# Optimization experiments

Measured on AMD Instinct MI355X. Metric: run time of the kernel, lower is better.

The kernel has to match this reference:

```python
import jax, jax.numpy as jnp
import numpy as np

N, C, D, H, E, M = 4, 512, 768, 12, 20, 4   # docs, seq, hidden, heads, entities/doc, max mentions
EMB, BLK, L = 768, 64, 97                    # emb_size, block_size, num_labels
P = E * (E - 1)                              # ordered entity pairs per doc
NEG = -1e30


def _forward(seq, attn, mention_start, hts, Wm1, Wm2, bm, Watt, batt, Wpath, bpath,
             Whead, bhead, Wtail, btail, Wbil, bbil):
    def per_doc(seq_i, att_i, pos0, ht):
        pos = pos0 + 1                                            # BERT cls offset
        e_emb = seq_i[pos]                                        # [E,M,D] mention embeddings
        mean_att = att_i.mean(0)                                  # [C,C] head-mean attention
        e_att = jnp.pad(mean_att[pos], ((0, 0), (0, 0), (0, 1)))  # [E,M,C+1] zero pad col
        glob = jax.nn.logsumexp(e_emb, axis=1)                    # [E,D] entity glob emb
        hidx, tidx = ht[:, 0], ht[:, 1]
        hs = e_emb[hidx]; ts = e_emb[tidx]                        # [P,M,D]
        h_att = e_att[hidx]; t_att = e_att[tidx]                  # [P,M,C+1]
        ph = pos[hidx]; pt = pos[tidx]                            # [P,M]
        idx_t = jnp.broadcast_to(pt[:, None, :], (P, M, M))
        idx_h = jnp.broadcast_to(ph[:, None, :], (P, M, M))
        pair_hatt = jnp.take_along_axis(h_att, idx_t, axis=2).mean(1)  # [P,M]
        pair_tatt = jnp.take_along_axis(t_att, idx_h, axis=2).mean(1)
        pair_hatt = pair_hatt / (pair_hatt.sum(1, keepdims=True) + 1e-5)
        pair_tatt = pair_tatt / (pair_tatt.sum(1, keepdims=True) + 1e-5)
        new_hs = jnp.einsum('pm,pmd->pd', pair_tatt, hs)
        new_ts = jnp.einsum('pm,pmd->pd', pair_hatt, ts)
        nh_att = jnp.einsum('pm,pmc->pc', pair_tatt, h_att)
        nt_att = jnp.einsum('pm,pmc->pc', pair_hatt, t_att)
        pa = nh_att * nt_att
        pa = pa / (pa.sum(1, keepdims=True) + 1e-5)
        rs = pa[:, :C] @ seq_i                                    # [P,D] local context
        # RelEdgeLayer over fully-connected entity graph (eval-mode dropout = identity)
        A = glob @ Wm1; B = glob @ Wm2
        edge = jax.nn.relu(A[:, None, :] + B[None, :, :] + bm)    # [E,E,D] edge features
        # path attention: query = cat(hs,ts), targets = cat(e[h,v],e[v,t],e[t,v],e[v,h])
        q = jnp.concatenate([new_hs, new_ts], -1)                 # [P,2D]
        qW = q @ Watt                                             # [P,4D] bilinear half
        q1, q2, q3, q4 = jnp.split(qW, 4, axis=-1)
        E1 = edge[hidx]                                           # edge[h,v]  [P,E,D]
        E2 = jnp.swapaxes(edge[:, tidx], 0, 1)                    # edge[v,t]
        E3 = edge[tidx]                                           # edge[t,v]
        E4 = jnp.swapaxes(edge[:, hidx], 0, 1)                    # edge[v,h]
        score = (jnp.einsum('pd,pvd->pv', q1, E1) + jnp.einsum('pd,pvd->pv', q2, E2)
                 + jnp.einsum('pd,pvd->pv', q3, E3) + jnp.einsum('pd,pvd->pv', q4, E4) + batt)
        v_ids = jnp.arange(E)
        mask = (v_ids[None, :] == hidx[:, None]) | (v_ids[None, :] == tidx[:, None])
        aw = jax.nn.softmax(jnp.where(mask, NEG, score), axis=-1)  # [P,E]
        path = jnp.concatenate([jnp.einsum('pv,pvd->pd', aw, Ek) for Ek in (E1, E2, E3, E4)], -1)
        return new_hs, new_ts, rs, path

    nh, nt, rs, path = jax.vmap(per_doc)(seq, attn, mention_start, hts)
    nh = nh.reshape(-1, D); nt = nt.reshape(-1, D)
    rs = rs.reshape(-1, D); path = path.reshape(-1, 4 * D)
    path = jax.nn.relu(path @ Wpath + bpath)
    hs = jax.nn.relu(jnp.concatenate([nh, rs, path], -1) @ Whead + bhead)
    ts = jax.nn.relu(jnp.concatenate([nt, rs, path], -1) @ Wtail + btail)
    b1 = hs.reshape(-1, EMB // BLK, BLK)
    b2 = ts.reshape(-1, EMB // BLK, BLK)
    bl = (b1[:, :, :, None] * b2[:, :, None, :]).reshape(-1, EMB * BLK)
    return bl @ Wbil + bbil                                       # [N*P, L] logits


def setup_inputs() -> dict:
    key = jax.random.key(0)
    ks = jax.random.split(key, 16)
    s = 0.02
    pairs = np.array([(i, j) for i in range(E) for j in range(E) if i != j], dtype=np.int32)
    return {
        'sequence_output': jax.random.normal(ks[0], (N, C, D), jnp.float32),
        'attention': jax.random.uniform(ks[1], (N, H, C, C), jnp.float32),
        'mention_start': jax.random.randint(ks[2], (N, E, M), 0, C - 2),
        'hts': jnp.broadcast_to(jnp.asarray(pairs), (N, P, 2)),
        'Wm1': jax.random.normal(ks[3], (D, D)) * s,
        'Wm2': jax.random.normal(ks[4], (D, D)) * s,
        'bm': jnp.zeros((D,), jnp.float32),
        'Watt': jax.random.normal(ks[5], (2 * D, 4 * D)) * s,
        'batt': jnp.zeros((), jnp.float32),
        'Wpath': jax.random.normal(ks[6], (4 * D, D)) * s,
        'bpath': jnp.zeros((D,), jnp.float32),
        'Whead': jax.random.normal(ks[7], (3 * D, EMB)) * s,
        'bhead': jnp.zeros((EMB,), jnp.float32),
        'Wtail': jax.random.normal(ks[8], (3 * D, EMB)) * s,
        'btail': jnp.zeros((EMB,), jnp.float32),
        'Wbil': jax.random.normal(ks[9], (EMB * BLK, L)) * s,
        'bbil': jnp.zeros((L,), jnp.float32),
    }


def reference(sequence_output, attention, mention_start, hts, Wm1, Wm2, bm, Watt, batt,
              Wpath, bpath, Whead, bhead, Wtail, btail, Wbil, bbil):
    return _forward(sequence_output, attention, mention_start, hts, Wm1, Wm2, bm, Watt,
                    batt, Wpath, bpath, Whead, bhead, Wtail, btail, Wbil, bbil)
```

## Files before the change

### kernel.cpp

```cpp
#include <hip/hip_runtime.h>
#include <hip/hip_bf16.h>

#define NDOC 4
#define CL   512
#define DD   768
#define HH   12
#define EE   20
#define MM   4
#define PP   380
#define NPAIR 1520
#define LOUT 97
#define KP   40

typedef unsigned short u16;
typedef short bf16x8 __attribute__((ext_vector_type(8)));
typedef u16   u16x8  __attribute__((ext_vector_type(8)));
typedef u16   u16x4  __attribute__((ext_vector_type(4)));
typedef float f32x4  __attribute__((ext_vector_type(4)));

#define Z8 (u16x8){0,0,0,0,0,0,0,0}

__device__ __forceinline__ u16 f2bf(float x){
    union { float f; unsigned u; } v; v.f = x;
    return (u16)((v.u + 0x7fffu + ((v.u >> 16) & 1u)) >> 16);
}
__device__ __forceinline__ float bf2f(u16 h){
    union { unsigned u; float f; } v; v.u = ((unsigned)h) << 16;
    return v.f;
}
__device__ __forceinline__ void splitf(float x, u16 &h, u16 &l){
    h = f2bf(x);
    l = f2bf(x - bf2f(h));
}
__device__ __forceinline__ void splitf_trunc(float x, u16 &h, u16 &l){
    union { float f; unsigned u; } v; v.f = x;
    h = (u16)(v.u >> 16);
    union { unsigned u; float f; } w; w.u = v.u & 0xffff0000u;
    union { float f; unsigned u; } s; s.f = x - w.f;
    l = (u16)(s.u >> 16);
}

__global__ __launch_bounds__(256) void k_wsplit(const float* __restrict__ W,
                                                u16* __restrict__ WH, u16* __restrict__ WL,
                                                int K, int N, long long srcStride,
                                                long long dstStride)
{
    __shared__ u16 tH[64][66], tL[64][66];
    const float* Wp = W + (size_t)blockIdx.z*srcStride;
    u16* WHp = WH + (size_t)blockIdx.z*dstStride;
    u16* WLp = WL + (size_t)blockIdx.z*dstStride;
    int n0 = blockIdx.x*64, k0 = blockIdx.y*64;
    int t = threadIdx.x;
    int kr = t>>4, c4 = (t&15)*4;
    bool vec4 = ((N & 3) == 0);
    #pragma unroll
    for (int rr=0; rr<4; ++rr) {
        int k = k0 + kr + rr*16;
        float arr[4];
        if (vec4 && n0 + c4 + 3 < N) {
            float4 v = *(const float4*)(Wp + (size_t)k*N + n0 + c4);
            arr[0]=v.x; arr[1]=v.y; arr[2]=v.z; arr[3]=v.w;
        } else {
            #pragma unroll
            for (int i=0;i<4;++i){ int n=n0+c4+i; arr[i] = (n<N)? Wp[(size_t)k*N+n] : 0.f; }
        }
        #pragma unroll
        for (int i=0;i<4;++i){
            u16 hh,ll; splitf(arr[i],hh,ll);
            tH[c4+i][kr+rr*16] = hh;
            tL[c4+i][kr+rr*16] = ll;
        }
    }
    __syncthreads();
    int nr = t>>4, kc = (t&15)*4;
    #pragma unroll
    for (int rr=0; rr<4; ++rr) {
        int nl = nr + rr*16;
        u16x4 vh, vl;
        #pragma unroll
        for (int i=0;i<4;++i){ vh[i]=tH[nl][kc+i]; vl[i]=tL[nl][kc+i]; }
        size_t o = (size_t)(n0+nl)*K + k0 + kc;
        *(u16x4*)(WHp + o) = vh;
        *(u16x4*)(WLp + o) = vl;
    }
}

__global__ __launch_bounds__(256) void k_prep(const float* __restrict__ att,
                                              const float* __restrict__ seq,
                                              const int* __restrict__ ms,
                                              float* __restrict__ eatt,
                                              float* __restrict__ glob)
{
    int b = blockIdx.x;
    if (b < NDOC*EE*MM) {
        int row = b;
        int i = row / (EE*MM);
        int pos = ms[row] + 1;
        const float* base = att + ((size_t)i*HH)*CL*CL + (size_t)pos*CL;
        for (int c = threadIdx.x; c < CL; c += 256) {
            float s = 0.f;
            #pragma unroll
            for (int h = 0; h < HH; ++h) s += base[(size_t)h*CL*CL + c];
            eatt[(size_t)row*CL + c] = s * (1.0f/HH);
        }
    } else {
        int ie = b - NDOC*EE*MM;
        int i = ie / EE;
        const int* mp = ms + ie*MM;
        const float* sb = seq + (size_t)i*CL*DD;
        const float* r0 = sb + (size_t)(mp[0]+1)*DD;
        const float* r1 = sb + (size_t)(mp[1]+1)*DD;
        const float* r2 = sb + (size_t)(mp[2]+1)*DD;
        const float* r3 = sb + (size_t)(mp[3]+1)*DD;
        for (int d = threadIdx.x; d < DD; d += 256) {
            float a=r0[d], bb=r1[d], c=r2[d], e=r3[d];
            float mx = fmaxf(fmaxf(a,bb), fmaxf(c,e));
            float s = expf(a-mx)+expf(bb-mx)+expf(c-mx)+expf(e-mx);
            glob[(size_t)ie*DD + d] = mx + logf(s);
        }
    }
}

__global__ __launch_bounds__(256) void k_pairvec(const float* __restrict__ seq,
                                                 const float* __restrict__ eatt,
                                                 const int* __restrict__ ms,
                                                 const int* __restrict__ hts,
                                                 u16* __restrict__ nhH, u16* __restrict__ nhL,
                                                 u16* __restrict__ ntH, u16* __restrict__ ntL,
                                                 u16* __restrict__ paH, u16* __restrict__ paL)
{
    int g = blockIdx.x;
    int i = g / PP;
    int h = hts[2*g], t = hts[2*g+1];
    const float* eh = eatt + (size_t)(i*EE+h)*MM*CL;
    const float* et = eatt + (size_t)(i*EE+t)*MM*CL;
    int ph[MM], pt[MM];
    #pragma unroll
    for (int m=0;m<MM;++m){ ph[m]=ms[(i*EE+h)*MM+m]+1; pt[m]=ms[(i*EE+t)*MM+m]+1; }
    float pH[MM], pT[MM]; float sh=0.f, st=0.f;
    #pragma unroll
    for (int m2=0; m2<MM; ++m2) {
        float s = 0.f, s2 = 0.f;
        #pragma unroll
        for (int m=0;m<MM;++m) { s += eh[m*CL + pt[m2]]; s2 += et[m*CL + ph[m2]]; }
        pH[m2] = s*0.25f;  sh += pH[m2];
        pT[m2] = s2*0.25f; st += pT[m2];
    }
    float rh = 1.f/(sh+1e-5f), rt = 1.f/(st+1e-5f);
    #pragma unroll
    for (int m=0;m<MM;++m){ pH[m]*=rh; pT[m]*=rt; }

    const float* sb = seq + (size_t)i*CL*DD;
    for (int d = threadIdx.x; d < DD; d += 256) {
        float nh = pT[0]*sb[(size_t)ph[0]*DD+d] + pT[1]*sb[(size_t)ph[1]*DD+d]
                 + pT[2]*sb[(size_t)ph[2]*DD+d] + pT[3]*sb[(size_t)ph[3]*DD+d];
        float nt = pH[0]*sb[(size_t)pt[0]*DD+d] + pH[1]*sb[(size_t)pt[1]*DD+d]
                 + pH[2]*sb[(size_t)pt[2]*DD+d] + pH[3]*sb[(size_t)pt[3]*DD+d];
        u16 hh,ll;
        splitf(nh,hh,ll);
        nhH[(size_t)g*DD + d]=hh; nhL[(size_t)g*DD + d]=ll;
        splitf(nt,hh,ll);
        ntH[(size_t)g*DD + d]=hh; ntL[(size_t)g*DD + d]=ll;
    }
    float vv[2]; float lsum = 0.f;
    #pragma unroll
    for (int it=0; it<2; ++it) {
        int c = threadIdx.x + it*256;
        float na = pT[0]*eh[c] + pT[1]*eh[CL+c] + pT[2]*eh[2*CL+c] + pT[3]*eh[3*CL+c];
        float nb = pH[0]*et[c] + pH[1]*et[CL+c] + pH[2]*et[2*CL+c] + pH[3]*et[3*CL+c];
        vv[it] = na*nb; lsum += vv[it];
    }
    float tot = lsum;
    #pragma unroll
    for (int o=32;o;o>>=1) tot += __shfl_xor(tot, o);
    __shared__ float wsum[4];
    if ((threadIdx.x & 63)==0) wsum[threadIdx.x>>6] = tot;
    __syncthreads();
    float inv = 1.f/(wsum[0]+wsum[1]+wsum[2]+wsum[3] + 1e-5f);
    #pragma unroll
    for (int it=0; it<2; ++it){
        int c = threadIdx.x + it*256;
        u16 hh,ll; splitf(vv[it]*inv,hh,ll);
        paH[(size_t)g*CL + c]=hh; paL[(size_t)g*CL + c]=ll;
    }
}

__global__ __launch_bounds__(256) void k_edge(const float* __restrict__ Ab,
                                              const float* __restrict__ Bb,
                                              const float* __restrict__ bm,
                                              float* __restrict__ edge)
{
    int iht = blockIdx.x;
    int i = iht/(EE*EE); int rem = iht%(EE*EE); int h = rem/EE; int tt = rem%EE;
    const float* a = Ab + (size_t)(i*EE+h)*DD;
    const float* b = Bb + (size_t)(i*EE+tt)*DD;
    float* e = edge + (size_t)iht*DD;
    for (int d=threadIdx.x; d<DD; d+=256)
        e[d] = fmaxf(a[d]+b[d]+bm[d], 0.f);
}

__global__ __launch_bounds__(256) void k_scorepath(const float* __restrict__ qW,
                                                   const float* __restrict__ edge,
                                                   const int* __restrict__ hts,
                                                   const float* __restrict__ battp,
                                                   u16* __restrict__ pathcH,
                                                   u16* __restrict__ pathcL)
{
    int g = blockIdx.x;
    int i = g / PP;
    int h = hts[2*g], t = hts[2*g+1];
    __shared__ float qs[4*DD];
    __shared__ float sc[EE];
    __shared__ float aw[EE];
    for (int d4 = threadIdx.x; d4 < DD; d4 += 256)
        *(float4*)&qs[d4*4] = *(const float4*)(qW + (size_t)g*3072 + d4*4);
    __syncthreads();
    const float* eb = edge + (size_t)i*EE*EE*DD;
    int lane = threadIdx.x & 63, wid = threadIdx.x >> 6;
    for (int v = wid; v < EE; v += 4) {
        const float* e1 = eb + (size_t)(h*EE+v)*DD;
        const float* e2 = eb + (size_t)(v*EE+t)*DD;
        const float* e3 = eb + (size_t)(t*EE+v)*DD;
        const float* e4 = eb + (size_t)(v*EE+h)*DD;
        float s = 0.f;
        for (int d = lane; d < DD; d += 64)
            s += qs[d]*e1[d] + qs[DD+d]*e2[d] + qs[2*DD+d]*e3[d] + qs[3*DD+d]*e4[d];
        #pragma unroll
        for (int o=32;o;o>>=1) s += __shfl_xor(s, o);
        if (lane==0) sc[v] = s + battp[0];
    }
    __syncthreads();
    if (threadIdx.x == 0) {
        float mx = -3.0e38f;
        for (int v=0;v<EE;++v){ float x = (v==h||v==t)? -1e30f : sc[v]; sc[v]=x; mx = fmaxf(mx,x); }
        float su=0.f;
        for (int v=0;v<EE;++v){ float e = expf(sc[v]-mx); aw[v]=e; su+=e; }
        float inv = 1.f/su;
        for (int v=0;v<EE;++v) aw[v]*=inv;
    }
    __syncthreads();
    for (int idx = threadIdx.x; idx < 4*DD; idx += 256) {
        int k = idx / DD, d = idx % DD;
        const float* e;
        int stride;
        if (k==0)      { e = eb + (size_t)h*EE*DD + d; stride = DD; }
        else if (k==1) { e = eb + (size_t)t*DD + d;     stride = EE*DD; }
        else if (k==2) { e = eb + (size_t)t*EE*DD + d;  stride = DD; }
        else           { e = eb + (size_t)h*DD + d;     stride = EE*DD; }
        float s = 0.f;
        #pragma unroll
        for (int v=0; v<EE; ++v) s += aw[v]*e[(size_t)v*stride];
        u16 hh,ll; splitf(s,hh,ll);
        pathcH[(size_t)g*3072 + idx] = hh;
        pathcL[(size_t)g*3072 + idx] = ll;
    }
}

__global__ __launch_bounds__(256) void gemm_f32s(const float* __restrict__ A, int lda, long long sA,
                                                 const float* __restrict__ B, int ldb,
                                                 float* __restrict__ C, int ldc, long long sC,
                                                 int M, int N, int K)
{
    int bz = blockIdx.z;
    A += (size_t)bz*sA;  C += (size_t)bz*sC;
    __shared__ float As[16][68];
    __shared__ float Bs[16][68];
    int m0 = blockIdx.y*64, n0 = blockIdx.x*64;
    int t = threadIdx.x;
    int tx = t & 15, ty = t >> 4;
    int am = t >> 2, ac = (t & 3) * 4;
    int bk = t >> 4, bn = (t & 15) * 4;
    float acc[4][4] = {};
    for (int k0 = 0; k0 < K; k0 += 16) {
        float4 av = make_float4(0,0,0,0);
        int gm = m0 + am;
        if (gm < M) av = *reinterpret_cast<const float4*>(A + (size_t)gm*lda + k0 + ac);
        As[ac+0][am]=av.x; As[ac+1][am]=av.y; As[ac+2][am]=av.z; As[ac+3][am]=av.w;
        float4 bv = *reinterpret_cast<const float4*>(B + (size_t)(k0+bk)*ldb + n0 + bn);
        *reinterpret_cast<float4*>(&Bs[bk][bn]) = bv;
        __syncthreads();
        #pragma unroll
        for (int kk=0; kk<16; ++kk) {
            const float4 a = *reinterpret_cast<const float4*>(&As[kk][ty*4]);
            const float4 b = *reinterpret_cast<const float4*>(&Bs[kk][tx*4]);
            float ar[4] = {a.x,a.y,a.z,a.w};
            float br[4] = {b.x,b.y,b.z,b.w};
            #pragma unroll
            for (int r=0;r<4;++r)
                #pragma unroll
                for (int c2=0;c2<4;++c2) acc[r][c2] = fmaf(ar[r], br[c2], acc[r][c2]);
        }
        __syncthreads();
    }
    #pragma unroll
    for (int r=0;r<4;++r) {
        int gm = m0 + ty*4 + r;
        if (gm >= M) continue;
        #pragma unroll
        for (int c2=0;c2<4;++c2)
            C[(size_t)gm*ldc + n0 + tx*4 + c2] = acc[r][c2];
    }
}

enum { MQW=0, MSPLIT=1, MRS=2, MBIL=3 };

template<int MODE, int BM, int BN>
__global__ __launch_bounds__(256) void gemm_mfma(
    const u16* __restrict__ aH0, const u16* __restrict__ aL0,
    const u16* __restrict__ aH1, const u16* __restrict__ aL1,
    const u16* __restrict__ aH2, const u16* __restrict__ aL2,
    const u16* __restrict__ bH, const u16* __restrict__ bL,
    const float* __restrict__ bias,
    float* __restrict__ oF,
    u16* __restrict__ oH, u16* __restrict__ oL,
    int M, int N, int Ktot, int segsz)
{
    constexpr int NWN = BN/64;
    constexpr int NWM = 4/NWN;
    constexpr int WM  = BM/NWM;
    constexpr int MFR = WM/16;
    constexpr int NFR = 4;
    __shared__ u16 AsH[BM*KP], AsL[BM*KP], BsH[BN*KP], BsL[BN*KP];

    const int t = threadIdx.x;
    const int z = blockIdx.z;
    const int m0 = blockIdx.y*BM, n0 = blockIdx.x*BN;
    const int lane = t & 63, wid = t >> 6;
    const int wr = wid / NWN, wc = wid % NWN;
    const int lrow = lane & 15, lg = lane >> 4;

    const u16 *segH0=aH0, *segL0=aL0;
    const u16 *bHp = bH, *bLp = bL;
    int Mloc = M;
    long long outRow0 = 0;
    if constexpr (MODE==MRS) {
        segH0 = aH0 + (size_t)z*PP*CL;  segL0 = aL0 + (size_t)z*PP*CL;
        bHp   = bH  + (size_t)z*DD*CL;  bLp   = bL  + (size_t)z*DD*CL;
        Mloc = PP; outRow0 = (long long)z*PP;
    }

    f32x4 acc[MFR][NFR];
    #pragma unroll
    for (int i=0;i<MFR;++i)
        #pragma unroll
        for (int j=0;j<NFR;++j) acc[i][j] = f32x4{0.f,0.f,0.f,0.f};

    const int kbase = (MODE==MBIL) ? z*2048 : 0;
    const int nkt   = ((MODE==MBIL) ? 2048 : Ktot) / 32;

    for (int kt = 0; kt < nkt; ++kt) {
        const int k0 = kbase + kt*32;
        if constexpr (MODE==MBIL) {
            int row = t>>2, koff = (t&3)*8;
            int gm = m0 + row;
            int k = k0 + koff;
            int hscol = k >> 6;
            int tscol = ((k >> 12) << 6) + (k & 63);
            u16x8 hv = Z8, lv = Z8;
            if (gm < Mloc) {
                float hsv = bf2f(aH0[(size_t)gm*DD + hscol]) + bf2f(aL0[(size_t)gm*DD + hscol]);
                u16x8 th = *(const u16x8*)(aH1 + (size_t)gm*DD + tscol);
                u16x8 tl = *(const u16x8*)(aL1 + (size_t)gm*DD + tscol);
                #pragma unroll
                for (int i2=0;i2<8;++i2){
                    float pr = hsv * (bf2f(th[i2]) + bf2f(tl[i2]));
                    u16 hh,ll; splitf_trunc(pr,hh,ll);
                    hv[i2]=hh; lv[i2]=ll;
                }
            }
            *(u16x8*)&AsH[row*KP + koff] = hv;
            *(u16x8*)&AsL[row*KP + koff] = lv;
        } else {
            int seg = (k0 >= 2*segsz) ? 2 : (k0 >= segsz ? 1 : 0);
            int soff = k0 - seg*segsz;
            const u16* pH = (seg==0)?segH0:(seg==1)?aH1:aH2;
            const u16* pL = (seg==0)?segL0:(seg==1)?aL1:aL2;
            if constexpr (BM==128) {
                int row = t>>1, koff = (t&1)*16;
                int gm = m0 + row;
                u16x8 h0=Z8,h1=Z8,l0=Z8,l1=Z8;
                if (gm < Mloc) {
                    const u16* ph = pH + (size_t)gm*segsz + soff + koff;
                    const u16* pl = pL + (size_t)gm*segsz + soff + koff;
                    h0 = *(const u16x8*)ph;  h1 = *(const u16x8*)(ph+8);
                    l0 = *(const u16x8*)pl;  l1 = *(const u16x8*)(pl+8);
                }
                *(u16x8*)&AsH[row*KP + koff]     = h0;
                *(u16x8*)&AsH[row*KP + koff + 8] = h1;
                *(u16x8*)&AsL[row*KP + koff]     = l0;
                *(u16x8*)&AsL[row*KP + koff + 8] = l1;
            } else {
                int row = t>>2, koff = (t&3)*8;
                int gm = m0 + row;
                u16x8 h0=Z8,l0=Z8;
                if (gm < Mloc) {
                    h0 = *(const u16x8*)(pH + (size_t)gm*segsz + soff + koff);
                    l0 = *(const u16x8*)(pL + (size_t)gm*segsz + soff + koff);
                }
                *(u16x8*)&AsH[row*KP + koff] = h0;
                *(u16x8*)&AsL[row*KP + koff] = l0;
            }
        }
        {
            if constexpr (BN==128) {
                int row = t>>1, koff = (t&1)*16;
                const u16* ph = bHp + (size_t)(n0+row)*Ktot + k0 + koff;
                const u16* pl = bLp + (size_t)(n0+row)*Ktot + k0 + koff;
                *(u16x8*)&BsH[row*KP + koff]     = *(const u16x8*)ph;
                *(u16x8*)&BsH[row*KP + koff + 8] = *(const u16x8*)(ph+8);
                *(u16x8*)&BsL[row*KP + koff]     = *(const u16x8*)pl;
                *(u16x8*)&BsL[row*KP + koff + 8] = *(const u16x8*)(pl+8);
            } else {
                int row = t>>2, koff = (t&3)*8;
                *(u16x8*)&BsH[row*KP + koff] = *(const u16x8*)(bHp + (size_t)(n0+row)*Ktot + k0 + koff);
                *(u16x8*)&BsL[row*KP + koff] = *(const u16x8*)(bLp + (size_t)(n0+row)*Ktot + k0 + koff);
            }
        }
        __syncthreads();
        {
            bf16x8 ah[MFR], al[MFR], bh[NFR], bl[NFR];
            #pragma unroll
            for (int mi=0;mi<MFR;++mi){
                int off = (wr*WM + mi*16 + lrow)*KP + lg*8;
                ah[mi] = *(const bf16x8*)&AsH[off];
                al[mi] = *(const bf16x8*)&AsL[off];
            }
            #pragma unroll
            for (int ni=0;ni<NFR;++ni){
                int off = (wc*64 + ni*16 + lrow)*KP + lg*8;
                bh[ni] = *(const bf16x8*)&BsH[off];
                bl[ni] = *(const bf16x8*)&BsL[off];
            }
            #pragma unroll
            for (int mi=0;mi<MFR;++mi)
                #pragma unroll
                for (int ni=0;ni<NFR;++ni){
                    acc[mi][ni] = __builtin_amdgcn_mfma_f32_16x16x32_bf16(ah[mi], bh[ni], acc[mi][ni], 0,0,0);
                    acc[mi][ni] = __builtin_amdgcn_mfma_f32_16x16x32_bf16(al[mi], bh[ni], acc[mi][ni], 0,0,0);
                    acc[mi][ni] = __builtin_amdgcn_mfma_f32_16x16x32_bf16(ah[mi], bl[ni], acc[mi][ni], 0,0,0);
                }
        }
        __syncthreads();
    }
    #pragma unroll
    for (int mi=0;mi<MFR;++mi)
        #pragma unroll
        for (int ni=0;ni<NFR;++ni)
            #pragma unroll
            for (int r=0;r<4;++r){
                int gm = m0 + wr*WM + mi*16 + lg*4 + r;
                int gn = n0 + wc*64 + ni*16 + lrow;
                if (gm >= Mloc) continue;
                float v = acc[mi][ni][r];
                if constexpr (MODE==MQW) {
                    oF[(size_t)gm*N + gn] = v;
                } else if constexpr (MODE==MSPLIT) {
                    v = fmaxf(v + bias[gn], 0.f);
                    u16 hh,ll; splitf(v,hh,ll);
                    oH[(size_t)gm*DD + gn] = hh;
                    oL[(size_t)gm*DD + gn] = ll;
                } else if constexpr (MODE==MRS) {
                    u16 hh,ll; splitf(v,hh,ll);
                    oH[(size_t)(outRow0+gm)*DD + gn] = hh;
                    oL[(size_t)(outRow0+gm)*DD + gn] = ll;
                } else {
                    if (gn < N) oF[((size_t)z*NPAIR + gm)*LOUT + gn] = v;
                }
            }
}

__global__ __launch_bounds__(256) void k_bilred(const float* __restrict__ partial,
                                                const float* __restrict__ bbil,
                                                float* __restrict__ out)
{
    int idx = blockIdx.x*blockDim.x + threadIdx.x;
    if (idx >= NPAIR*LOUT) return;
    int l = idx % LOUT;
    float s = bbil[l];
    #pragma unroll 4
    for (int sl=0; sl<24; ++sl) s += partial[(size_t)sl*NPAIR*LOUT + idx];
    out[idx] = s;
}

extern "C" void kernel_launch(void* const* d_in, const int* in_sizes, int n_in,
                              void* d_out, int out_size, void* d_ws, size_t ws_size,
                              hipStream_t stream)
{
    (void)in_sizes; (void)n_in; (void)out_size;
    const float* seq   = (const float*)d_in[0];
    const float* att   = (const float*)d_in[1];
    const int*   ms    = (const int*)d_in[2];
    const int*   hts   = (const int*)d_in[3];
    const float* Wm1   = (const float*)d_in[4];
    const float* Wm2   = (const float*)d_in[5];
    const float* bm    = (const float*)d_in[6];
    const float* Watt  = (const float*)d_in[7];
    const float* batt  = (const float*)d_in[8];
    const float* Wpath = (const float*)d_in[9];
    const float* bpath = (const float*)d_in[10];
    const float* Whead = (const float*)d_in[11];
    const float* bhead = (const float*)d_in[12];
    const float* Wtail = (const float*)d_in[13];
    const float* btail = (const float*)d_in[14];
    const float* Wbil  = (const float*)d_in[15];
    const float* bbil  = (const float*)d_in[16];
    float* out = (float*)d_out;

    char* base = (char*)d_ws;
    size_t off = 0;
    auto take = [&](size_t bytes)->char* { char* r = base+off; off += bytes; return r; };
    char*  R0      = base;
    float* edge    = (float*)take(4915200);
    float* qWb     = (float*)take(18677760);
    u16*   pathcH  = (u16*)  take(9338880);
    u16*   pathcL  = (u16*)  take(9338880);
    u16* nhH = (u16*)take(2334720);  u16* nhL = (u16*)take(2334720);
    u16* ntH = (u16*)take(2334720);  u16* ntL = (u16*)take(2334720);
    u16* rsH = (u16*)take(2334720);  u16* rsL = (u16*)take(2334720);
    u16* pthH= (u16*)take(2334720);  u16* pthL= (u16*)take(2334720);
    u16* hsH = (u16*)take(2334720);  u16* hsL = (u16*)take(2334720);
    u16* tsH = (u16*)take(2334720);  u16* tsL = (u16*)take(2334720);
    float* glob = (float*)take(245760);
    float* Abuf = (float*)take(245760);
    float* Bbuf = (float*)take(245760);
    char*  R1     = base+off;
    float* eatt   = (float*)take(655360);
    u16*   paH    = (u16*)  take(1556480);
    u16*   paL    = (u16*)  take(1556480);
    u16*   seqTH  = (u16*)  take(3145728);
    u16*   seqTL  = (u16*)  take(3145728);
    char*  R2     = base+off;
    u16*   WattTH = (u16*)  take(9437184);
    u16*   WattTL = (u16*)  take(9437184);
    size_t peak = off;
    if (peak > ws_size) return;

    u16* WpathTH = (u16*)R1;
    u16* WpathTL = (u16*)(R1 + 4718592);
    u16* WheadTH = (u16*)R2;
    u16* WheadTL = (u16*)(R2 + 3538944);
    u16* WtailTH = (u16*)(R2 + 7077888);
    u16* WtailTL = (u16*)(R2 + 10616832);
    float* part  = (float*)R2;
    u16* WbilTH  = (u16*)R0;
    u16* WbilTL  = (u16*)(R0 + 12582912);

    k_wsplit<<<dim3(3072/64, 1536/64, 1), 256, 0, stream>>>(Watt, WattTH, WattTL, 1536, 3072, 0, 0);
    k_wsplit<<<dim3(768/64, 512/64, NDOC), 256, 0, stream>>>(seq, seqTH, seqTL, 512, 768,
                                                             (long long)CL*DD, (long long)DD*CL);
    k_prep<<<NDOC*EE*MM + NDOC*EE, 256, 0, stream>>>(att, seq, ms, eatt, glob);
    k_pairvec<<<NPAIR, 256, 0, stream>>>(seq, eatt, ms, hts, nhH, nhL, ntH, ntL, paH, paL);

    gemm_f32s<<<dim3(12, 1, NDOC), 256, 0, stream>>>(glob, DD, (long long)EE*DD, Wm1, DD,
                                                     Abuf, DD, (long long)EE*DD, EE, DD, DD);
    gemm_f32s<<<dim3(12, 1, NDOC), 256, 0, stream>>>(glob, DD, (long long)EE*DD, Wm2, DD,
                                                     Bbuf, DD, (long long)EE*DD, EE, DD, DD);
    k_edge<<<NDOC*EE*EE, 256, 0, stream>>>(Abuf, Bbuf, bm, edge);

    gemm_mfma<MRS,64,64><<<dim3(12, 6, NDOC), 256, 0, stream>>>(
        paH, paL, nullptr, nullptr, nullptr, nullptr, seqTH, seqTL, nullptr,
        nullptr, rsH, rsL, PP, DD, CL, CL);

    k_wsplit<<<dim3(768/64, 3072/64, 1), 256, 0, stream>>>(Wpath, WpathTH, WpathTL, 3072, 768, 0, 0);

    gemm_mfma<MQW,128,128><<<dim3(3072/128, 12, 1), 256, 0, stream>>>(
        nhH, nhL, ntH, ntL, nullptr, nullptr, WattTH, WattTL, nullptr,
        qWb, nullptr, nullptr, NPAIR, 3072, 1536, DD);

    k_wsplit<<<dim3(768/64, 2304/64, 1), 256, 0, stream>>>(Whead, WheadTH, WheadTL, 2304, 768, 0, 0);
    k_wsplit<<<dim3(768/64, 2304/64, 1), 256, 0, stream>>>(Wtail, WtailTH, WtailTL, 2304, 768, 0, 0);

    k_scorepath<<<NPAIR, 256, 0, stream>>>(qWb, edge, hts, batt, pathcH, pathcL);

    gemm_mfma<MSPLIT,64,64><<<dim3(12, 24, 1), 256, 0, stream>>>(
        pathcH, pathcL, nullptr, nullptr, nullptr, nullptr, WpathTH, WpathTL, bpath,
        nullptr, pthH, pthL, NPAIR, DD, 3072, 3072);

    k_wsplit<<<dim3(128/64, 49152/64, 1), 256, 0, stream>>>(Wbil, WbilTH, WbilTL, 49152, LOUT, 0, 0);

    gemm_mfma<MSPLIT,64,64><<<dim3(12, 24, 1), 256, 0, stream>>>(
        nhH, nhL, rsH, rsL, pthH, pthL, WheadTH, WheadTL, bhead,
        nullptr, hsH, hsL, NPAIR, DD, 2304, DD);
    gemm_mfma<MSPLIT,64,64><<<dim3(12, 24, 1), 256, 0, stream>>>(
        ntH, ntL, rsH, rsL, pthH, pthL, WtailTH, WtailTL, btail,
        nullptr, tsH, tsL, NPAIR, DD, 2304, DD);

    gemm_mfma<MBIL,64,128><<<dim3(1, 24, 24), 256, 0, stream>>>(
        hsH, hsL, tsH, tsL, nullptr, nullptr, WbilTH, WbilTL, nullptr,
        part, nullptr, nullptr, NPAIR, LOUT, 49152, 49152);

    k_bilred<<<(NPAIR*LOUT+255)/256, 256, 0, stream>>>(part, bbil, out);
}
```

Measured before the change: 775.6 us.

## Factor bilinear as per-head-column GEMM over tail, scale by head, atomics

```diff
diff --git a/kernel.cpp b/kernel.cpp
--- a/kernel.cpp
+++ b/kernel.cpp
@@ -11,6 +11,7 @@
 #define NPAIR 1520
 #define LOUT 97
 #define KP   40
+#define KP2  72
 
 typedef unsigned short u16;
 typedef short bf16x8 __attribute__((ext_vector_type(8)));
@@ -31,13 +32,6 @@
 __device__ __forceinline__ void splitf(float x, u16 &h, u16 &l){
     h = f2bf(x);
     l = f2bf(x - bf2f(h));
-}
-__device__ __forceinline__ void splitf_trunc(float x, u16 &h, u16 &l){
-    union { float f; unsigned u; } v; v.f = x;
-    h = (u16)(v.u >> 16);
-    union { unsigned u; float f; } w; w.u = v.u & 0xffff0000u;
-    union { float f; unsigned u; } s; s.f = x - w.f;
-    l = (u16)(s.u >> 16);
 }
 
 __global__ __launch_bounds__(256) void k_wsplit(const float* __restrict__ W,
@@ -256,27 +250,29 @@
     }
 }
 
-__global__ __launch_bounds__(256) void gemm_f32s(const float* __restrict__ A, int lda, long long sA,
-                                                 const float* __restrict__ B, int ldb,
-                                                 float* __restrict__ C, int ldc, long long sC,
-                                                 int M, int N, int K)
-{
-    int bz = blockIdx.z;
-    A += (size_t)bz*sA;  C += (size_t)bz*sC;
+__global__ __launch_bounds__(256) void gemm_f32s(const float* __restrict__ glob,
+                                                 const float* __restrict__ W1,
+                                                 const float* __restrict__ W2,
+                                                 float* __restrict__ C1,
+                                                 float* __restrict__ C2)
+{
+    int doc = blockIdx.z >> 1, sel = blockIdx.z & 1;
+    const float* A = glob + (size_t)doc*EE*DD;
+    const float* B = sel ? W2 : W1;
+    float* C = (sel ? C2 : C1) + (size_t)doc*EE*DD;
     __shared__ float As[16][68];
     __shared__ float Bs[16][68];
-    int m0 = blockIdx.y*64, n0 = blockIdx.x*64;
+    int n0 = blockIdx.x*64;
     int t = threadIdx.x;
     int tx = t & 15, ty = t >> 4;
     int am = t >> 2, ac = (t & 3) * 4;
     int bk = t >> 4, bn = (t & 15) * 4;
     float acc[4][4] = {};
-    for (int k0 = 0; k0 < K; k0 += 16) {
+    for (int k0 = 0; k0 < DD; k0 += 16) {
         float4 av = make_float4(0,0,0,0);
-        int gm = m0 + am;
-        if (gm < M) av = *reinterpret_cast<const float4*>(A + (size_t)gm*lda + k0 + ac);
+        if (am < EE) av = *reinterpret_cast<const float4*>(A + (size_t)am*DD + k0 + ac);
         As[ac+0][am]=av.x; As[ac+1][am]=av.y; As[ac+2][am]=av.z; As[ac+3][am]=av.w;
-        float4 bv = *reinterpret_cast<const float4*>(B + (size_t)(k0+bk)*ldb + n0 + bn);
+        float4 bv = *reinterpret_cast<const float4*>(B + (size_t)(k0+bk)*DD + n0 + bn);
         *reinterpret_cast<float4*>(&Bs[bk][bn]) = bv;
         __syncthreads();
         #pragma unroll
@@ -294,25 +290,28 @@
     }
     #pragma unroll
     for (int r=0;r<4;++r) {
-        int gm = m0 + ty*4 + r;
-        if (gm >= M) continue;
+        int gm = ty*4 + r;
+        if (gm >= EE) continue;
         #pragma unroll
         for (int c2=0;c2<4;++c2)
-            C[(size_t)gm*ldc + n0 + tx*4 + c2] = acc[r][c2];
-    }
-}
-
-enum { MQW=0, MSPLIT=1, MRS=2, MBIL=3 };
+            C[(size_t)gm*DD + n0 + tx*4 + c2] = acc[r][c2];
+    }
+}
+
+enum { MQW=0, MSPLIT=1, MRS=2, MHT=3 };
 
 template<int MODE, int BM, int BN>
 __global__ __launch_bounds__(256) void gemm_mfma(
     const u16* __restrict__ aH0, const u16* __restrict__ aL0,
     const u16* __restrict__ aH1, const u16* __restrict__ aL1,
     const u16* __restrict__ aH2, const u16* __restrict__ aL2,
+    const u16* __restrict__ a0bH, const u16* __restrict__ a0bL,
     const u16* __restrict__ bH, const u16* __restrict__ bL,
-    const float* __restrict__ bias,
+    const u16* __restrict__ bHb, const u16* __restrict__ bLb,
+    const float* __restrict__ bias, const float* __restrict__ biasb,
     float* __restrict__ oF,
     u16* __restrict__ oH, u16* __restrict__ oL,
+    u16* __restrict__ oHb, u16* __restrict__ oLb,
     int M, int N, int Ktot, int segsz)
 {
     constexpr int NWN = BN/64;
@@ -331,6 +330,9 @@
 
     const u16 *segH0=aH0, *segL0=aL0;
     const u16 *bHp = bH, *bLp = bL;
+    const float* bp = bias;
+    float* fOut = nullptr;
+    u16 *hOut = oH, *lOut = oL;
     int Mloc = M;
     long long outRow0 = 0;
     if constexpr (MODE==MRS) {
@@ -338,6 +340,11 @@
         bHp   = bH  + (size_t)z*DD*CL;  bLp   = bL  + (size_t)z*DD*CL;
         Mloc = PP; outRow0 = (long long)z*PP;
     }
+    if constexpr (MODE==MHT) {
+        if (z == 0) { fOut = oF; hOut = nullptr; lOut = nullptr; }
+        else { segH0 = a0bH; segL0 = a0bL; bHp = bHb; bLp = bLb; bp = biasb;
+               hOut = oHb; lOut = oLb; }
+    }
 
     f32x4 acc[MFR][NFR];
     #pragma unroll
@@ -345,32 +352,11 @@
         #pragma unroll
         for (int j=0;j<NFR;++j) acc[i][j] = f32x4{0.f,0.f,0.f,0.f};
 
-    const int kbase = (MODE==MBIL) ? z*2048 : 0;
-    const int nkt   = ((MODE==MBIL) ? 2048 : Ktot) / 32;
+    const int nkt = Ktot / 32;
 
     for (int kt = 0; kt < nkt; ++kt) {
-        const int k0 = kbase + kt*32;
-        if constexpr (MODE==MBIL) {
-            int row = t>>2, koff = (t&3)*8;
-            int gm = m0 + row;
-            int k = k0 + koff;
-            int hscol = k >> 6;
-            int tscol = ((k >> 12) << 6) + (k & 63);
-            u16x8 hv = Z8, lv = Z8;
-            if (gm < Mloc) {
-                float hsv = bf2f(aH0[(size_t)gm*DD + hscol]) + bf2f(aL0[(size_t)gm*DD + hscol]);
-                u16x8 th = *(const u16x8*)(aH1 + (size_t)gm*DD + tscol);
-                u16x8 tl = *(const u16x8*)(aL1 + (size_t)gm*DD + tscol);
-                #pragma unroll
-                for (int i2=0;i2<8;++i2){
-                    float pr = hsv * (bf2f(th[i2]) + bf2f(tl[i2]));
-                    u16 hh,ll; splitf_trunc(pr,hh,ll);
-                    hv[i2]=hh; lv[i2]=ll;
-                }
-            }
-            *(u16x8*)&AsH[row*KP + koff] = hv;
-            *(u16x8*)&AsL[row*KP + koff] = lv;
-        } else {
+        const int k0 = kt*32;
+        {
             int seg = (k0 >= 2*segsz) ? 2 : (k0 >= segsz ? 1 : 0);
             int soff = k0 - seg*segsz;
             const u16* pH = (seg==0)?segH0:(seg==1)?aH1:aH2;
@@ -454,32 +440,141 @@
                 float v = acc[mi][ni][r];
                 if constexpr (MODE==MQW) {
                     oF[(size_t)gm*N + gn] = v;
-                } else if constexpr (MODE==MSPLIT) {
-                    v = fmaxf(v + bias[gn], 0.f);
-                    u16 hh,ll; splitf(v,hh,ll);
-                    oH[(size_t)gm*DD + gn] = hh;
-                    oL[(size_t)gm*DD + gn] = ll;
                 } else if constexpr (MODE==MRS) {
                     u16 hh,ll; splitf(v,hh,ll);
                     oH[(size_t)(outRow0+gm)*DD + gn] = hh;
                     oL[(size_t)(outRow0+gm)*DD + gn] = ll;
                 } else {
-                    if (gn < N) oF[((size_t)z*NPAIR + gm)*LOUT + gn] = v;
+                    v = fmaxf(v + bp[gn], 0.f);
+                    if (fOut) fOut[(size_t)gm*DD + gn] = v;
+                    if (hOut) {
+                        u16 hh,ll; splitf(v,hh,ll);
+                        hOut[(size_t)gm*DD + gn] = hh;
+                        lOut[(size_t)gm*DD + gn] = ll;
+                    }
                 }
             }
 }
 
-__global__ __launch_bounds__(256) void k_bilred(const float* __restrict__ partial,
-                                                const float* __restrict__ bbil,
-                                                float* __restrict__ out)
+__global__ __launch_bounds__(256) void k_bil2(const u16* __restrict__ tsH,
+                                              const u16* __restrict__ tsL,
+                                              const float* __restrict__ hsF,
+                                              const u16* __restrict__ WH,
+                                              const u16* __restrict__ WL,
+                                              float* __restrict__ out)
+{
+    __shared__ u16 TsH[128*KP2], TsL[128*KP2];
+    __shared__ u16 BbH[128*KP], BbL[128*KP];
+    const int t = threadIdx.x;
+    const int m0 = blockIdx.y*128;
+    const int z = blockIdx.z;
+    const int j = z>>2, a0 = (z&3)*16;
+    const int lane = t & 63, wid = t >> 6;
+    const int wr = wid >> 1, wc = wid & 1;
+    const int lrow = lane & 15, lg = lane >> 4;
+
+    {
+        int row = t>>1, half = t&1;
+        int gm = m0 + row;
+        int col = j*64 + half*32;
+        u16x8 h0=Z8,h1=Z8,h2=Z8,h3=Z8,l0=Z8,l1=Z8,l2=Z8,l3=Z8;
+        if (gm < NPAIR) {
+            const u16* ph = tsH + (size_t)gm*DD + col;
+            const u16* pl = tsL + (size_t)gm*DD + col;
+            h0=*(const u16x8*)ph;      h1=*(const u16x8*)(ph+8);
+            h2=*(const u16x8*)(ph+16); h3=*(const u16x8*)(ph+24);
+            l0=*(const u16x8*)pl;      l1=*(const u16x8*)(pl+8);
+            l2=*(const u16x8*)(pl+16); l3=*(const u16x8*)(pl+24);
+        }
+        int o = row*KP2 + half*32;
+        *(u16x8*)&TsH[o]=h0;    *(u16x8*)&TsH[o+8]=h1;
+        *(u16x8*)&TsH[o+16]=h2; *(u16x8*)&TsH[o+24]=h3;
+        *(u16x8*)&TsL[o]=l0;    *(u16x8*)&TsL[o+8]=l1;
+        *(u16x8*)&TsL[o+16]=l2; *(u16x8*)&TsL[o+24]=l3;
+    }
+
+    f32x4 facc[4][4];
+    #pragma unroll
+    for (int mi=0;mi<4;++mi)
+        #pragma unroll
+        for (int ni=0;ni<4;++ni) facc[mi][ni] = f32x4{0.f,0.f,0.f,0.f};
+
+    for (int ai=0; ai<16; ++ai) {
+        int a = a0 + ai;
+        f32x4 tacc[4][4];
+        #pragma unroll
+        for (int mi=0;mi<4;++mi)
+            #pragma unroll
+            for (int ni=0;ni<4;++ni) tacc[mi][ni] = f32x4{0.f,0.f,0.f,0.f};
+        #pragma unroll
+        for (int half=0; half<2; ++half) {
+            __syncthreads();
+            {
+                int row = t>>1, h2 = t&1;
+                size_t src = (size_t)row*49152 + (size_t)j*4096 + (size_t)a*64 + half*32 + h2*16;
+                *(u16x8*)&BbH[row*KP + h2*16]     = *(const u16x8*)(WH + src);
+                *(u16x8*)&BbH[row*KP + h2*16 + 8] = *(const u16x8*)(WH + src + 8);
+                *(u16x8*)&BbL[row*KP + h2*16]     = *(const u16x8*)(WL + src);
+                *(u16x8*)&BbL[row*KP + h2*16 + 8] = *(const u16x8*)(WL + src + 8);
+            }
+            __syncthreads();
+            bf16x8 ah[4], al[4], bh[4], bl[4];
+            #pragma unroll
+            for (int mi=0;mi<4;++mi){
+                int off = (wr*64 + mi*16 + lrow)*KP2 + half*32 + lg*8;
+                ah[mi] = *(const bf16x8*)&TsH[off];
+                al[mi] = *(const bf16x8*)&TsL[off];
+            }
+            #pragma unroll
+            for (int ni=0;ni<4;++ni){
+                int off = (wc*64 + ni*16 + lrow)*KP + lg*8;
+                bh[ni] = *(const bf16x8*)&BbH[off];
+                bl[ni] = *(const bf16x8*)&BbL[off];
+            }
+            #pragma unroll
+            for (int mi=0;mi<4;++mi)
+                #pragma unroll
+                for (int ni=0;ni<4;++ni){
+                    tacc[mi][ni] = __builtin_amdgcn_mfma_f32_16x16x32_bf16(ah[mi], bh[ni], tacc[mi][ni], 0,0,0);
+                    tacc[mi][ni] = __builtin_amdgcn_mfma_f32_16x16x32_bf16(al[mi], bh[ni], tacc[mi][ni], 0,0,0);
+                    tacc[mi][ni] = __builtin_amdgcn_mfma_f32_16x16x32_bf16(ah[mi], bl[ni], tacc[mi][ni], 0,0,0);
+                }
+        }
+        float hv[4][4];
+        #pragma unroll
+        for (int mi=0;mi<4;++mi)
+            #pragma unroll
+            for (int r=0;r<4;++r){
+                int gm = m0 + wr*64 + mi*16 + lg*4 + r;
+                hv[mi][r] = (gm < NPAIR) ? hsF[(size_t)gm*DD + j*64 + a] : 0.f;
+            }
+        #pragma unroll
+        for (int mi=0;mi<4;++mi)
+            #pragma unroll
+            for (int ni=0;ni<4;++ni)
+                #pragma unroll
+                for (int r=0;r<4;++r)
+                    facc[mi][ni][r] = fmaf(hv[mi][r], tacc[mi][ni][r], facc[mi][ni][r]);
+    }
+    #pragma unroll
+    for (int mi=0;mi<4;++mi)
+        #pragma unroll
+        for (int ni=0;ni<4;++ni)
+            #pragma unroll
+            for (int r=0;r<4;++r){
+                int gm = m0 + wr*64 + mi*16 + lg*4 + r;
+                int gn = wc*64 + ni*16 + lrow;
+                if (gm < NPAIR && gn < LOUT)
+                    atomicAdd(&out[(size_t)gm*LOUT + gn], facc[mi][ni][r]);
+            }
+}
+
+__global__ __launch_bounds__(256) void k_outinit(const float* __restrict__ bbil,
+                                                 float* __restrict__ out)
 {
     int idx = blockIdx.x*blockDim.x + threadIdx.x;
     if (idx >= NPAIR*LOUT) return;
-    int l = idx % LOUT;
-    float s = bbil[l];
-    #pragma unroll 4
-    for (int sl=0; sl<24; ++sl) s += partial[(size_t)sl*NPAIR*LOUT + idx];
-    out[idx] = s;
+    out[idx] = bbil[idx % LOUT];
 }
 
 extern "C" void kernel_launch(void* const* d_in, const int* in_sizes, int n_in,
@@ -518,8 +613,8 @@
     u16* ntH = (u16*)take(2334720);  u16* ntL = (u16*)take(2334720);
     u16* rsH = (u16*)take(2334720);  u16* rsL = (u16*)take(2334720);
     u16* pthH= (u16*)take(2334720);  u16* pthL= (u16*)take(2334720);
-    u16* hsH = (u16*)take(2334720);  u16* hsL = (u16*)take(2334720);
     u16* tsH = (u16*)take(2334720);  u16* tsL = (u16*)take(2334720);
+    float* hsF = (float*)take(4669440);
     float* glob = (float*)take(245760);
     float* Abuf = (float*)take(245760);
     float* Bbuf = (float*)take(245760);
@@ -541,7 +636,6 @@
     u16* WheadTL = (u16*)(R2 + 3538944);
     u16* WtailTH = (u16*)(R2 + 7077888);
     u16* WtailTL = (u16*)(R2 + 10616832);
-    float* part  = (float*)R2;
     u16* WbilTH  = (u16*)R0;
     u16* WbilTL  = (u16*)(R0 + 12582912);
 
@@ -551,21 +645,21 @@
     k_prep<<<NDOC*EE*MM + NDOC*EE, 256, 0, stream>>>(att, seq, ms, eatt, glob);
     k_pairvec<<<NPAIR, 256, 0, stream>>>(seq, eatt, ms, hts, nhH, nhL, ntH, ntL, paH, paL);
 
-    gemm_f32s<<<dim3(12, 1, NDOC), 256, 0, stream>>>(glob, DD, (long long)EE*DD, Wm1, DD,
-                                                     Abuf, DD, (long long)EE*DD, EE, DD, DD);
-    gemm_f32s<<<dim3(12, 1, NDOC), 256, 0, stream>>>(glob, DD, (long long)EE*DD, Wm2, DD,
-                                                     Bbuf, DD, (long long)EE*DD, EE, DD, DD);
+    gemm_f32s<<<dim3(12, 1, 2*NDOC), 256, 0, stream>>>(glob, Wm1, Wm2, Abuf, Bbuf);
     k_edge<<<NDOC*EE*EE, 256, 0, stream>>>(Abuf, Bbuf, bm, edge);
+    k_outinit<<<(NPAIR*LOUT+255)/256, 256, 0, stream>>>(bbil, out);
 
     gemm_mfma<MRS,64,64><<<dim3(12, 6, NDOC), 256, 0, stream>>>(
-        paH, paL, nullptr, nullptr, nullptr, nullptr, seqTH, seqTL, nullptr,
-        nullptr, rsH, rsL, PP, DD, CL, CL);
+        paH, paL, nullptr, nullptr, nullptr, nullptr, nullptr, nullptr,
+        seqTH, seqTL, nullptr, nullptr, nullptr, nullptr,
+        nullptr, rsH, rsL, nullptr, nullptr, PP, DD, CL, CL);
 
     k_wsplit<<<dim3(768/64, 3072/64, 1), 256, 0, stream>>>(Wpath, WpathTH, WpathTL, 3072, 768, 0, 0);
 
     gemm_mfma<MQW,128,128><<<dim3(3072/128, 12, 1), 256, 0, stream>>>(
-        nhH, nhL, ntH, ntL, nullptr, nullptr, WattTH, WattTL, nullptr,
-        qWb, nullptr, nullptr, NPAIR, 3072, 1536, DD);
+        nhH, nhL, ntH, ntL, nullptr, nullptr, nullptr, nullptr,
+        WattTH, WattTL, nullptr, nullptr, nullptr, nullptr,
+        qWb, nullptr, nullptr, nullptr, nullptr, NPAIR, 3072, 1536, DD);
 
     k_wsplit<<<dim3(768/64, 2304/64, 1), 256, 0, stream>>>(Whead, WheadTH, WheadTL, 2304, 768, 0, 0);
     k_wsplit<<<dim3(768/64, 2304/64, 1), 256, 0, stream>>>(Wtail, WtailTH, WtailTL, 2304, 768, 0, 0);
@@ -573,21 +667,16 @@
     k_scorepath<<<NPAIR, 256, 0, stream>>>(qWb, edge, hts, batt, pathcH, pathcL);
 
     gemm_mfma<MSPLIT,64,64><<<dim3(12, 24, 1), 256, 0, stream>>>(
-        pathcH, pathcL, nullptr, nullptr, nullptr, nullptr, WpathTH, WpathTL, bpath,
-        nullptr, pthH, pthL, NPAIR, DD, 3072, 3072);
+        pathcH, pathcL, nullptr, nullptr, nullptr, nullptr, nullptr, nullptr,
+        WpathTH, WpathTL, nullptr, nullptr, bpath, nullptr,
+        nullptr, pthH, pthL, nullptr, nullptr, NPAIR, DD, 3072, 3072);
 
     k_wsplit<<<dim3(128/64, 49152/64, 1), 256, 0, stream>>>(Wbil, WbilTH, WbilTL, 49152, LOUT, 0, 0);
 
-    gemm_mfma<MSPLIT,64,64><<<dim3(12, 24, 1), 256, 0, stream>>>(
-        nhH, nhL, rsH, rsL, pthH, pthL, WheadTH, WheadTL, bhead,
-        nullptr, hsH, hsL, NPAIR, DD, 2304, DD);
-    gemm_mfma<MSPLIT,64,64><<<dim3(12, 24, 1), 256, 0, stream>>>(
-        ntH, ntL, rsH, rsL, pthH, pthL, WtailTH, WtailTL, btail,
-        nullptr, tsH, tsL, NPAIR, DD, 2304, DD);
-
-    gemm_mfma<MBIL,64,128><<<dim3(1, 24, 24), 256, 0, stream>>>(
-        hsH, hsL, tsH, tsL, nullptr, nullptr, WbilTH, WbilTL, nullptr,
-        part, nullptr, nullptr, NPAIR, LOUT, 49152, 49152);
-
-    k_bilred<<<(NPAIR*LOUT+255)/256, 256, 0, stream>>>(part, bbil, out);
-}
+    gemm_mfma<MHT,64,64><<<dim3(12, 24, 2), 256, 0, stream>>>(
+        nhH, nhL, rsH, rsL, pthH, pthL, ntH, ntL,
+        WheadTH, WheadTL, WtailTH, WtailTL, bhead, btail,
+        hsF, nullptr, nullptr, tsH, tsL, NPAIR, DD, 2304, DD);
+
+    k_bil2<<<dim3(1, 12, 48), 256, 0, stream>>>(tsH, tsL, hsF, WbilTH, WbilTL, out);
+}
```

Result: faster. 726.8 us (-6.3%).
